# Kernel optimization log

Hardware: AMD Instinct MI355X
Metric: run time of the kernel (lower is better)

## Reference

```python
import jax, jax.numpy as jnp
import numpy as np

EPS = 1e-6
NEG = 1e9

def _norm(x):
    # Normalizator math with alpha=1, gamma=0 (torch.std is unbiased -> ddof=1)
    m = jnp.mean(x, axis=-1, keepdims=True)
    s = jnp.std(x, axis=-1, ddof=1, keepdims=True)
    return (x - m) / (s + EPS)

def setup_inputs() -> dict:
    key = jax.random.key(0)
    ks = jax.random.split(key, 16)
    T, S, D, F, L = 4096, 4096, 512, 2048, 4
    sc = 1.0 / np.sqrt(D)
    scf = 1.0 / np.sqrt(F)
    return {
        "current_tgt_output": jax.random.normal(ks[0], (T, D), jnp.float32),
        "encoder_output": jax.random.normal(ks[1], (S, D), jnp.float32),
        "cross_mask": jax.random.randint(ks[2], (T, S), 0, 2).astype(jnp.float32),
        "Wq": jax.random.normal(ks[3], (L, D, D), jnp.float32) * sc,
        "Wk": jax.random.normal(ks[4], (L, D, D), jnp.float32) * sc,
        "Wv": jax.random.normal(ks[5], (L, D, D), jnp.float32) * sc,
        "Wo": jax.random.normal(ks[6], (L, D, D), jnp.float32) * sc,
        "Cq": jax.random.normal(ks[7], (L, D, D), jnp.float32) * sc,
        "Ck": jax.random.normal(ks[8], (L, D, D), jnp.float32) * sc,
        "Cv": jax.random.normal(ks[9], (L, D, D), jnp.float32) * sc,
        "Co": jax.random.normal(ks[10], (L, D, D), jnp.float32) * sc,
        "W1": jax.random.normal(ks[11], (L, D, F), jnp.float32) * sc,
        "W2": jax.random.normal(ks[12], (L, F, D), jnp.float32) * scf,
        "alpha": jnp.ones((1,), jnp.float32),
        "gamma": jnp.zeros((1,), jnp.float32),
        "input_ids": jax.random.randint(ks[13], (T,), 0, S),
        "training_step": T,
        "training_mode": 1,
    }

def reference(current_tgt_output, encoder_output, cross_mask, Wq, Wk, Wv, Wo,
              Cq, Ck, Cv, Co, W1, W2, alpha, gamma, input_ids,
              training_step, training_mode):
    T = training_step
    x = current_tgt_output[:T] if training_mode else current_tgt_output
    cm = cross_mask[:T]                                  # [T, S]
    # the python double-loop -> single vectorized gather: self_mask[i,k]=cross_mask[i, input_ids[k]]
    self_mask = cm[:, input_ids]                         # [T, T]
    sbias = (self_mask - 1.0) * NEG                      # additive mask bias
    cbias = (cm - 1.0) * NEG
    D = x.shape[-1]
    scale = 1.0 / jnp.sqrt(jnp.asarray(D, x.dtype))
    L = Wq.shape[0]
    for l in range(L):
        h = _norm(x)
        q, k, v = h @ Wq[l], h @ Wk[l], h @ Wv[l]
        a = jax.nn.softmax(q @ k.T * scale + sbias, axis=-1)
        x = x + (a @ v) @ Wo[l]
        h = _norm(x)
        q = h @ Cq[l]
        k, v = encoder_output @ Ck[l], encoder_output @ Cv[l]
        a = jax.nn.softmax(q @ k.T * scale + cbias, axis=-1)
        x = x + (a @ v) @ Co[l]
        h = _norm(x)
        x = x + jax.nn.relu(h @ W1[l]) @ W2[l]
    return alpha * _norm(x) + gamma
```

## Files before the change

### kernel.cpp

```cpp
#include <hip/hip_runtime.h>
#include <math.h>

typedef _Float16 half_t;
typedef unsigned int u32;
typedef unsigned short u16;
typedef float f32x4 __attribute__((ext_vector_type(4)));
typedef _Float16 f16x8 __attribute__((ext_vector_type(8)));
typedef _Float16 f16x4 __attribute__((ext_vector_type(4)));

#define T_DIM 4096
#define S_DIM 4096
#define D_DIM 512
#define F_DIM 2048
#define NLAYER 4
#define KVS ((size_t)4096 * 512)

__device__ __forceinline__ void gload16(const void* g, void* l) {
    __builtin_amdgcn_global_load_lds(
        (const __attribute__((address_space(1))) u32*)g,
        (__attribute__((address_space(3))) u32*)l, 16, 0, 0);
}

template<int N> __device__ __forceinline__ void wait_vm() {
    if constexpr (N == 0) asm volatile("s_waitcnt vmcnt(0)" ::: "memory");
    else if constexpr (N == 3) asm volatile("s_waitcnt vmcnt(3)" ::: "memory");
    else if constexpr (N == 4) asm volatile("s_waitcnt vmcnt(4)" ::: "memory");
    else if constexpr (N == 6) asm volatile("s_waitcnt vmcnt(6)" ::: "memory");
    else if constexpr (N == 8) asm volatile("s_waitcnt vmcnt(8)" ::: "memory");
}

template<int BN, int EPI>
__global__ __launch_bounds__(512)
void gemm_nt(const half_t* __restrict__ A, int lda,
             const half_t* __restrict__ B, int ldb,
             int N, int K, int gx,
             half_t* __restrict__ D1, half_t* __restrict__ D2,
             half_t* __restrict__ D3, int ldd)
{
    constexpr int BM = 128, BK = 64;
    constexpr int NF = BN / 32;
    constexpr int LPT = 2 + BN / 64;
    constexpr int NSLOT = (BN == 64) ? 3 : 2;
    __shared__ half_t As[NSLOT][BM * BK];
    __shared__ half_t Bs[NSLOT][BN * BK];

    const int tid  = threadIdx.x;
    const int wave = tid >> 6;
    const int lane = tid & 63;

    const int nb  = gridDim.x;
    const int bid = blockIdx.x;
    const int nid = (bid & 7) * (nb >> 3) + (bid >> 3);
    const int bx  = nid % gx;
    const int by  = nid / gx;
    const int bm = by * BM, bn = bx * BN;

    const int wm = (wave >> 1) * 32;
    const int wn = (wave & 1) * (BN / 2);
    const int kq = lane >> 4;
    const int rr = lane & 15;
    const int scol = (((lane & 7) ^ (lane >> 3)) << 3);

    f32x4 acc[2][NF];
#pragma unroll
    for (int m = 0; m < 2; ++m)
#pragma unroll
        for (int n = 0; n < NF; ++n)
            acc[m][n] = f32x4{0.f, 0.f, 0.f, 0.f};

    auto stage = [&](int buf, int k0) {
#pragma unroll
        for (int c = 0; c < 2; ++c) {
            const int row = wave * 16 + c * 8 + (lane >> 3);
            gload16(A + (size_t)(bm + row) * lda + k0 + scol,
                    (char*)&As[buf][0] + (wave * 2 + c) * 1024 + lane * 16);
        }
        if constexpr (BN == 64) {
            const int row = wave * 8 + (lane >> 3);
            gload16(B + (size_t)(bn + row) * ldb + k0 + scol,
                    (char*)&Bs[buf][0] + wave * 1024 + lane * 16);
        } else {
#pragma unroll
            for (int c = 0; c < 2; ++c) {
                const int row = wave * 16 + c * 8 + (lane >> 3);
                gload16(B + (size_t)(bn + row) * ldb + k0 + scol,
                        (char*)&Bs[buf][0] + (wave * 2 + c) * 1024 + lane * 16);
            }
        }
    };

    const int nt = K / BK;
    stage(0, 0);
    if constexpr (NSLOT == 3) stage(1, BK);
    int cur = 0, pf = NSLOT - 1;
    for (int t = 0; t < nt; ++t) {
        if (t + 1 < nt) wait_vm<(NSLOT - 2) * LPT>(); else wait_vm<0>();
        __builtin_amdgcn_s_barrier();
        if (t + NSLOT - 1 < nt) stage(pf, (t + NSLOT - 1) * BK);
#pragma unroll
        for (int ks = 0; ks < 2; ++ks) {
            f16x8 af[2], bf[NF];
#pragma unroll
            for (int m = 0; m < 2; ++m) {
                const int r = wm + m * 16 + rr;
                af[m] = *(const f16x8*)&As[cur][r * BK + (((ks * 4 + kq) ^ (r & 7)) << 3)];
            }
#pragma unroll
            for (int n = 0; n < NF; ++n) {
                const int r = wn + n * 16 + rr;
                bf[n] = *(const f16x8*)&Bs[cur][r * BK + (((ks * 4 + kq) ^ (r & 7)) << 3)];
            }
#pragma unroll
            for (int m = 0; m < 2; ++m)
#pragma unroll
                for (int n = 0; n < NF; ++n)
                    acc[m][n] = __builtin_amdgcn_mfma_f32_16x16x32_f16(af[m], bf[n], acc[m][n], 0, 0, 0);
        }
        cur = (cur + 1 == NSLOT) ? 0 : cur + 1;
        pf  = (pf  + 1 == NSLOT) ? 0 : pf  + 1;
    }

    const int r0 = bm + wm + (lane >> 4) * 4;
#pragma unroll
    for (int m = 0; m < 2; ++m)
#pragma unroll
        for (int n = 0; n < NF; ++n) {
            const int c = bn + wn + n * 16 + rr;
            if (EPI == 2) {
#pragma unroll
                for (int i = 0; i < 4; ++i)
                    D1[(size_t)(r0 + m * 16 + i) * ldd + c] = (half_t)acc[m][n][i];
            } else if (EPI == 5) {
                half_t* Dst = (bn < 512) ? D1 : (bn < 1024) ? D2 : D3;
                const int sub = c & 511;
#pragma unroll
                for (int i = 0; i < 4; ++i)
                    Dst[(size_t)(r0 + m * 16 + i) * 512 + sub] = (half_t)acc[m][n][i];
            } else {
                const int l = c >> 10;
                const int sub = c & 1023;
                half_t* Dst = (sub < 512) ? (D2 + l * KVS) : (D3 + l * KVS);
                const int d = sub & 511;
#pragma unroll
                for (int i = 0; i < 4; ++i)
                    Dst[(size_t)(r0 + m * 16 + i) * 512 + d] = (half_t)acc[m][n][i];
            }
        }
}

__global__ __launch_bounds__(512)
void gemm_fold(const half_t* __restrict__ Wt, const half_t* __restrict__ V,
               half_t* __restrict__ Out, int zSA, long zSB, long zSD)
{
    constexpr int BM = 128, BK = 64, BN = 64, NSLOT = 3, LPT = 3;
    __shared__ half_t As[NSLOT][BM * BK];
    __shared__ half_t Bs[NSLOT][BN * BK];

    const half_t* A = Wt + (size_t)blockIdx.z * zSA;
    const half_t* B = V  + (size_t)blockIdx.z * zSB;
    half_t* D = Out + (size_t)blockIdx.z * zSD;

    const int tid  = threadIdx.x;
    const int wave = tid >> 6;
    const int lane = tid & 63;

    const int nb  = gridDim.x;
    const int bid = blockIdx.x;
    const int nid = (bid & 7) * (nb >> 3) + (bid >> 3);
    const int bx = nid & 63, by = nid >> 6;
    const int bm = by * BM, bn = bx * BN;

    const int wm = (wave >> 1) * 32;
    const int wn = (wave & 1) * 32;
    const int kq = lane >> 4;
    const int rr = lane & 15;
    const int scol = (((lane & 7) ^ (lane >> 3)) << 3);

    f32x4 acc[2][2];
#pragma unroll
    for (int m = 0; m < 2; ++m)
#pragma unroll
        for (int n = 0; n < 2; ++n)
            acc[m][n] = f32x4{0.f, 0.f, 0.f, 0.f};

    auto stage = [&](int buf, int k0) {
#pragma unroll
        for (int c = 0; c < 2; ++c) {
            const int row = wave * 16 + c * 8 + (lane >> 3);
            gload16(A + (size_t)(bm + row) * 512 + k0 + scol,
                    (char*)&As[buf][0] + (wave * 2 + c) * 1024 + lane * 16);
        }
        const int row = wave * 8 + (lane >> 3);
        gload16(B + (size_t)(bn + row) * 512 + k0 + scol,
                (char*)&Bs[buf][0] + wave * 1024 + lane * 16);
    };

    const int nt = 512 / BK;
    stage(0, 0);
    stage(1, BK);
    int cur = 0, pf = 2;
    for (int t = 0; t < nt; ++t) {
        if (t + 1 < nt) wait_vm<LPT>(); else wait_vm<0>();
        __builtin_amdgcn_s_barrier();
        if (t + 2 < nt) stage(pf, (t + 2) * BK);
#pragma unroll
        for (int ks = 0; ks < 2; ++ks) {
            f16x8 af[2], bf[2];
#pragma unroll
            for (int m = 0; m < 2; ++m) {
                const int r = wm + m * 16 + rr;
                af[m] = *(const f16x8*)&As[cur][r * BK + (((ks * 4 + kq) ^ (r & 7)) << 3)];
            }
#pragma unroll
            for (int n = 0; n < 2; ++n) {
                const int r = wn + n * 16 + rr;
                bf[n] = *(const f16x8*)&Bs[cur][r * BK + (((ks * 4 + kq) ^ (r & 7)) << 3)];
            }
#pragma unroll
            for (int m = 0; m < 2; ++m)
#pragma unroll
                for (int n = 0; n < 2; ++n)
                    acc[m][n] = __builtin_amdgcn_mfma_f32_16x16x32_f16(af[m], bf[n], acc[m][n], 0, 0, 0);
        }
        cur = (cur + 1 == NSLOT) ? 0 : cur + 1;
        pf  = (pf  + 1 == NSLOT) ? 0 : pf  + 1;
    }

    const int r0 = bm + wm + (lane >> 4) * 4;
#pragma unroll
    for (int m = 0; m < 2; ++m)
#pragma unroll
        for (int n = 0; n < 2; ++n) {
            const int c = bn + wn + n * 16 + rr;
#pragma unroll
            for (int i = 0; i < 4; ++i)
                D[(size_t)(r0 + m * 16 + i) * 4096 + c] = (half_t)acc[m][n][i];
        }
}

template<int EPI, int SPLITK = 1, int P16 = 1>
__global__ __launch_bounds__(256)
void gemm97(const half_t* __restrict__ A, int lda,
            const half_t* __restrict__ B, int ldb,
            int K, int gx, half_t* __restrict__ D,
            float* __restrict__ Fout, int ldd)
{
    constexpr int BK = 32, NSLOT = 3, LPT = 4;
    __shared__ half_t As[NSLOT][128 * BK];
    __shared__ half_t Bs[NSLOT][128 * BK];

    const int tid  = threadIdx.x;
    const int wave = tid >> 6;
    const int lane = tid & 63;

    const int nb  = gridDim.x;
    const int bid = blockIdx.x;
    const int nid = (bid & 7) * (nb >> 3) + (bid >> 3);
    const int gy  = nb / (gx * SPLITK);
    const int bx  = nid % gx;
    const int tmp = nid / gx;
    const int by  = tmp % gy;
    const int kz  = tmp / gy;
    const int bm = by * 128, bn = bx * 128;

    const int Keff = K / SPLITK;
    A += (size_t)kz * Keff;
    B += (size_t)kz * Keff;

    const int wm = (wave >> 1) * 64;
    const int wn = (wave & 1) * 64;
    const int kq = lane >> 4;
    const int rr = lane & 15;
    const int srow = lane >> 2;
    const int scol = (((lane & 3) ^ ((lane >> 3) & 3)) << 3);
    const int kqa  = kq ^ ((rr >> 1) & 3);

    const half_t* Abase = A + (size_t)(bm + wave * 16 + srow) * lda + scol;
    const half_t* Bbase = B + (size_t)(bn + wave * 16 + srow) * ldb + scol;

    f32x4 acc[4][4];
#pragma unroll
    for (int m = 0; m < 4; ++m)
#pragma unroll
        for (int n = 0; n < 4; ++n)
            acc[m][n] = f32x4{0.f, 0.f, 0.f, 0.f};

    auto stage = [&](int buf, int k0) {
#pragma unroll
        for (int c = 0; c < 2; ++c)
            gload16(Abase + (size_t)c * 64 * lda + k0,
                    (char*)&As[buf][0] + c * 4096 + wave * 1024 + lane * 16);
#pragma unroll
        for (int c = 0; c < 2; ++c)
            gload16(Bbase + (size_t)c * 64 * ldb + k0,
                    (char*)&Bs[buf][0] + c * 4096 + wave * 1024 + lane * 16);
    };

    const int nt = Keff / BK;
    stage(0, 0);
    stage(1, BK);
    int cur = 0, pf = 2;
    for (int t = 0; t < nt; ++t) {
        if (t + 1 < nt) wait_vm<LPT>(); else wait_vm<0>();
        __builtin_amdgcn_s_barrier();
        if (t + 2 < nt) stage(pf, (t + 2) * BK);
        f16x8 af[4], bf[4];
#pragma unroll
        for (int m = 0; m < 4; ++m)
            af[m] = *(const f16x8*)&As[cur][(wm + m * 16 + rr) * BK + kqa * 8];
#pragma unroll
        for (int n = 0; n < 4; ++n)
            bf[n] = *(const f16x8*)&Bs[cur][(wn + n * 16 + rr) * BK + kqa * 8];
#pragma unroll
        for (int m = 0; m < 4; ++m)
#pragma unroll
            for (int n = 0; n < 4; ++n)
                acc[m][n] = __builtin_amdgcn_mfma_f32_16x16x32_f16(af[m], bf[n], acc[m][n], 0, 0, 0);
        cur = (cur == 2) ? 0 : cur + 1;
        pf  = (pf  == 2) ? 0 : pf + 1;
    }

    const int r0 = bm + wm + (lane >> 4) * 4;
    const int soff = kz * gx * 128;
#pragma unroll
    for (int m = 0; m < 4; ++m)
#pragma unroll
        for (int n = 0; n < 4; ++n) {
            const int c = bn + wn + n * 16 + rr;
#pragma unroll
            for (int i = 0; i < 4; ++i) {
                float v = acc[m][n][i];
                const size_t r = r0 + m * 16 + i;
                if constexpr (SPLITK > 1) {
                    if constexpr (P16) D[r * ldd + soff + c] = (half_t)v;
                    else               Fout[r * ldd + soff + c] = v;
                } else {
                    if (EPI == 4) v = fmaxf(v, 0.f);
                    D[r * ldd + c] = (half_t)v;
                }
            }
        }
}

__global__ __launch_bounds__(256)
void attn_tail(const float* __restrict__ xin, const half_t* __restrict__ P,
               float* __restrict__ xbuf, half_t* __restrict__ hh)
{
    const int row  = blockIdx.x * 4 + (threadIdx.x >> 6);
    const int lane = threadIdx.x & 63;
    const int d0 = lane * 8;
    float v[8];
    {
        const float* xr = xin + (size_t)row * D_DIM + d0;
        float4 a = *(const float4*)xr;
        float4 b = *(const float4*)(xr + 4);
        v[0]=a.x; v[1]=a.y; v[2]=a.z; v[3]=a.w; v[4]=b.x; v[5]=b.y; v[6]=b.z; v[7]=b.w;
    }
    const half_t* pr = P + (size_t)row * 2048 + d0;
#pragma unroll
    for (int j = 0; j < 4; ++j) {
        f16x8 pv = *(const f16x8*)(pr + j * 512);
#pragma unroll
        for (int e = 0; e < 8; ++e) v[e] += (float)pv[e];
    }
    float* xo = xbuf + (size_t)row * D_DIM + d0;
    *(float4*)xo       = float4{v[0], v[1], v[2], v[3]};
    *(float4*)(xo + 4) = float4{v[4], v[5], v[6], v[7]};

    float s = 0.f;
#pragma unroll
    for (int j = 0; j < 8; ++j) s += v[j];
#pragma unroll
    for (int off = 32; off; off >>= 1) s += __shfl_xor(s, off);
    const float mean = s * (1.f / 512.f);
    float ss = 0.f;
#pragma unroll
    for (int j = 0; j < 8; ++j) { float d = v[j] - mean; ss += d * d; }
#pragma unroll
    for (int off = 32; off; off >>= 1) ss += __shfl_xor(ss, off);
    const float inv = 1.f / (sqrtf(ss * (1.f / 511.f)) + 1e-6f);
    f16x8 hv;
#pragma unroll
    for (int j = 0; j < 8; ++j) hv[j] = (half_t)((v[j] - mean) * inv);
    *(f16x8*)&hh[(size_t)row * D_DIM + d0] = hv;
}

template<int FINAL>
__global__ __launch_bounds__(256)
void norm_red(const float* __restrict__ xin, const float* __restrict__ P,
              float* __restrict__ xbuf, half_t* __restrict__ hh,
              float* __restrict__ outF, const float* __restrict__ alphaP,
              const float* __restrict__ gammaP)
{
    const int row  = blockIdx.x * 4 + (threadIdx.x >> 6);
    const int lane = threadIdx.x & 63;
    const int d0 = lane * 8;
    const float* xr = xin + (size_t)row * D_DIM + d0;
    float v[8];
    {
        float4 a = *(const float4*)xr;
        float4 b = *(const float4*)(xr + 4);
        v[0]=a.x; v[1]=a.y; v[2]=a.z; v[3]=a.w; v[4]=b.x; v[5]=b.y; v[6]=b.z; v[7]=b.w;
    }
    const float* pr = P + (size_t)row * 2048 + d0;
#pragma unroll
    for (int j = 0; j < 4; ++j) {
        float4 a = *(const float4*)(pr + j * 512);
        float4 b = *(const float4*)(pr + j * 512 + 4);
        v[0]+=a.x; v[1]+=a.y; v[2]+=a.z; v[3]+=a.w; v[4]+=b.x; v[5]+=b.y; v[6]+=b.z; v[7]+=b.w;
    }
    if (!FINAL) {
        float* xo = xbuf + (size_t)row * D_DIM + d0;
        *(float4*)xo       = float4{v[0], v[1], v[2], v[3]};
        *(float4*)(xo + 4) = float4{v[4], v[5], v[6], v[7]};
    }
    float s = 0.f;
#pragma unroll
    for (int j = 0; j < 8; ++j) s += v[j];
#pragma unroll
    for (int off = 32; off; off >>= 1) s += __shfl_xor(s, off);
    const float mean = s * (1.f / 512.f);
    float ss = 0.f;
#pragma unroll
    for (int j = 0; j < 8; ++j) { float d = v[j] - mean; ss += d * d; }
#pragma unroll
    for (int off = 32; off; off >>= 1) ss += __shfl_xor(ss, off);
    const float inv = 1.f / (sqrtf(ss * (1.f / 511.f)) + 1e-6f);
    if (FINAL) {
        const float alp = alphaP[0], gam = gammaP[0];
        float o[8];
#pragma unroll
        for (int j = 0; j < 8; ++j) o[j] = alp * ((v[j] - mean) * inv) + gam;
        float* op = outF + (size_t)row * D_DIM + d0;
        *(float4*)op       = float4{o[0], o[1], o[2], o[3]};
        *(float4*)(op + 4) = float4{o[4], o[5], o[6], o[7]};
    } else {
        f16x8 hv;
#pragma unroll
        for (int j = 0; j < 8; ++j) hv[j] = (half_t)((v[j] - mean) * inv);
        *(f16x8*)&hh[(size_t)row * D_DIM + d0] = hv;
    }
}

template<int FINAL>
__global__ __launch_bounds__(256)
void norm_rows(const float* __restrict__ x, half_t* __restrict__ hh,
               float* __restrict__ outF, const float* __restrict__ alphaP,
               const float* __restrict__ gammaP)
{
    const int row  = blockIdx.x * 4 + (threadIdx.x >> 6);
    const int lane = threadIdx.x & 63;
    const float* xr = x + (size_t)row * D_DIM + lane * 8;
    float4 a = *(const float4*)xr;
    float4 b = *(const float4*)(xr + 4);
    float v[8] = {a.x, a.y, a.z, a.w, b.x, b.y, b.z, b.w};
    float s = 0.f;
#pragma unroll
    for (int j = 0; j < 8; ++j) s += v[j];
#pragma unroll
    for (int off = 32; off; off >>= 1) s += __shfl_xor(s, off);
    const float mean = s * (1.f / 512.f);
    float ss = 0.f;
#pragma unroll
    for (int j = 0; j < 8; ++j) { float d = v[j] - mean; ss += d * d; }
#pragma unroll
    for (int off = 32; off; off >>= 1) ss += __shfl_xor(ss, off);
    const float inv = 1.f / (sqrtf(ss * (1.f / 511.f)) + 1e-6f);
    if (FINAL) {
        const float alp = alphaP[0], gam = gammaP[0];
        float o[8];
#pragma unroll
        for (int j = 0; j < 8; ++j) o[j] = alp * ((v[j] - mean) * inv) + gam;
        float* op = outF + (size_t)row * D_DIM + lane * 8;
        *(float4*)op       = float4{o[0], o[1], o[2], o[3]};
        *(float4*)(op + 4) = float4{o[4], o[5], o[6], o[7]};
    } else {
        f16x8 hv;
#pragma unroll
        for (int j = 0; j < 8; ++j) hv[j] = (half_t)((v[j] - mean) * inv);
        *(f16x8*)&hh[(size_t)row * D_DIM + lane * 8] = hv;
    }
}

__global__ __launch_bounds__(256)
void cast_f16(const float* __restrict__ in, half_t* __restrict__ out)
{
    size_t i = ((size_t)blockIdx.x * 256 + threadIdx.x) * 8;
    float4 a = *(const float4*)&in[i];
    float4 b = *(const float4*)&in[i + 4];
    float v[8] = {a.x, a.y, a.z, a.w, b.x, b.y, b.z, b.w};
    f16x8 o;
#pragma unroll
    for (int j = 0; j < 8; ++j) o[j] = (half_t)v[j];
    *(f16x8*)&out[i] = o;
}

__global__ __launch_bounds__(256)
void transpose_cast(const float* __restrict__ in, half_t* __restrict__ out,
                    int R, int C, float scale, int inZ, int outZ)
{
    in  += (size_t)blockIdx.z * inZ;
    out += (size_t)blockIdx.z * outZ;
    __shared__ float tile[32][33];
    const int tx = threadIdx.x & 31, ty = threadIdx.x >> 5;
    const int r0 = blockIdx.y * 32, c0 = blockIdx.x * 32;
#pragma unroll
    for (int i = 0; i < 4; ++i)
        tile[ty + i * 8][tx] = in[(size_t)(r0 + ty + i * 8) * C + c0 + tx];
    __syncthreads();
#pragma unroll
    for (int i = 0; i < 4; ++i)
        out[(size_t)(c0 + ty + i * 8) * R + r0 + tx] = (half_t)(tile[tx][ty + i * 8] * scale);
}

__global__ __launch_bounds__(256)
void pack_masks(const float* __restrict__ cm, const int* __restrict__ ids,
                u32* __restrict__ crossb, u32* __restrict__ selfb)
{
    const int t = blockIdx.x;
    const float* row = cm + (size_t)t * S_DIM;
    __shared__ u32 cb[S_DIM / 32];
    __shared__ u16 sh16[256];
    const int tid = threadIdx.x;
    u32 bits = 0;
#pragma unroll
    for (int q = 0; q < 4; ++q) {
        float4 v = *(const float4*)&row[tid * 16 + q * 4];
        bits |= (v.x > 0.5f ? 1u : 0u) << (q * 4 + 0);
        bits |= (v.y > 0.5f ? 1u : 0u) << (q * 4 + 1);
        bits |= (v.z > 0.5f ? 1u : 0u) << (q * 4 + 2);
        bits |= (v.w > 0.5f ? 1u : 0u) << (q * 4 + 3);
    }
    ((u16*)cb)[tid] = (u16)bits;
    __syncthreads();
    u32 sb = 0;
#pragma unroll
    for (int q = 0; q < 4; ++q) {
        int4 id4 = *(const int4*)&ids[tid * 16 + q * 4];
        sb |= ((cb[id4.x >> 5] >> (id4.x & 31)) & 1u) << (q * 4 + 0);
        sb |= ((cb[id4.y >> 5] >> (id4.y & 31)) & 1u) << (q * 4 + 1);
        sb |= ((cb[id4.z >> 5] >> (id4.z & 31)) & 1u) << (q * 4 + 2);
        sb |= ((cb[id4.w >> 5] >> (id4.w & 31)) & 1u) << (q * 4 + 3);
    }
    sh16[tid] = (u16)sb;
    __syncthreads();
    if (tid < 128) {
        crossb[(size_t)t * 128 + tid] = cb[tid];
        selfb[(size_t)t * 128 + tid]  = (u32)sh16[2 * tid] | ((u32)sh16[2 * tid + 1] << 16);
    }
}

__global__ __launch_bounds__(256)
void softmax_rows16(half_t* __restrict__ logits, const u32* __restrict__ bits)
{
    const int t = blockIdx.x;
    half_t* row = logits + (size_t)t * S_DIM;
    const u32* bw = bits + (size_t)t * (S_DIM / 32);
    __shared__ float red[8];
    const int tid = threadIdx.x, wave = tid >> 6, lane = tid & 63;
    const int s0 = tid * 16;
    f16x8 h0 = *(const f16x8*)&row[s0];
    f16x8 h1 = *(const f16x8*)&row[s0 + 8];
    const u32 w = bw[tid >> 1] >> ((tid & 1) * 16);
    float z[16];
    float lmax = -3.0e38f;
#pragma unroll
    for (int q = 0; q < 16; ++q) {
        const float v = (float)((q < 8) ? h0[q & 7] : h1[q & 7]);
        z[q] = v + (((w >> q) & 1u) ? 0.f : -1e9f);
        lmax = fmaxf(lmax, z[q]);
    }
#pragma unroll
    for (int off = 32; off; off >>= 1) lmax = fmaxf(lmax, __shfl_xor(lmax, off));
    if (lane == 0) red[wave] = lmax;
    __syncthreads();
    const float mx = fmaxf(fmaxf(red[0], red[1]), fmaxf(red[2], red[3]));
    float lsum = 0.f;
#pragma unroll
    for (int q = 0; q < 16; ++q) { z[q] = __expf(z[q] - mx); lsum += z[q]; }
#pragma unroll
    for (int off = 32; off; off >>= 1) lsum += __shfl_xor(lsum, off);
    if (lane == 0) red[4 + wave] = lsum;
    __syncthreads();
    const float inv = 1.f / (red[4] + red[5] + red[6] + red[7]);
    f16x8 o0, o1;
#pragma unroll
    for (int q = 0; q < 8; ++q) {
        o0[q] = (half_t)(z[q] * inv);
        o1[q] = (half_t)(z[q + 8] * inv);
    }
    *(f16x8*)&row[s0] = o0;
    *(f16x8*)&row[s0 + 8] = o1;
}

extern "C" void kernel_launch(void* const* d_in, const int* in_sizes, int n_in,
                              void* d_out, int out_size, void* d_ws, size_t ws_size,
                              hipStream_t stream)
{
    (void)in_sizes; (void)n_in; (void)out_size; (void)ws_size;

    const float* x0p  = (const float*)d_in[0];
    const float* encp = (const float*)d_in[1];
    const float* cmp  = (const float*)d_in[2];
    const float* Wq = (const float*)d_in[3], *Wk = (const float*)d_in[4];
    const float* Wv = (const float*)d_in[5], *Wo = (const float*)d_in[6];
    const float* Cq = (const float*)d_in[7], *Ck = (const float*)d_in[8];
    const float* Cv = (const float*)d_in[9], *Co = (const float*)d_in[10];
    const float* W1p = (const float*)d_in[11];
    const float* W2p = (const float*)d_in[12];
    const float* alphap = (const float*)d_in[13];
    const float* gammap = (const float*)d_in[14];
    const int*   idsp   = (const int*)d_in[15];
    float* outp = (float*)d_out;

    char* wp = (char*)d_ws;
    auto take = [&](size_t nelem, int esz) -> void* {
        void* p = (void*)wp;
        wp += (nelem * (size_t)esz + 255) & ~(size_t)255;
        return p;
    };
    half_t* wqkvT = (half_t*)take((size_t)NLAYER * 1536 * 512, 2);
    half_t* ckvT  = (half_t*)take((size_t)NLAYER * 1024 * 512, 2);
    half_t* cqT   = (half_t*)take((size_t)NLAYER * 512 * 512, 2);
    half_t* woT   = (half_t*)take((size_t)NLAYER * 512 * 512, 2);
    half_t* coT   = (half_t*)take((size_t)NLAYER * 512 * 512, 2);
    half_t* w1T   = (half_t*)take((size_t)NLAYER * D_DIM * F_DIM, 2);
    half_t* w2T   = (half_t*)take((size_t)NLAYER * D_DIM * F_DIM, 2);
    half_t* hh    = (half_t*)take((size_t)T_DIM * D_DIM, 2);
    half_t* qb    = (half_t*)take((size_t)T_DIM * D_DIM, 2);
    half_t* kb    = (half_t*)take((size_t)S_DIM * D_DIM, 2);
    half_t* vb    = (half_t*)take((size_t)S_DIM * D_DIM, 2);
    half_t* vTp   = (half_t*)take((size_t)S_DIM * D_DIM, 2);
    half_t* mid   = (half_t*)take((size_t)T_DIM * F_DIM, 2);
    half_t* enc16 = (half_t*)take((size_t)S_DIM * D_DIM, 2);
    half_t* kbC   = (half_t*)take((size_t)NLAYER * S_DIM * D_DIM, 2);
    half_t* vC    = (half_t*)take((size_t)NLAYER * S_DIM * D_DIM, 2);
    half_t* vTCp  = (half_t*)take((size_t)NLAYER * S_DIM * D_DIM, 2);
    float* xbuf   = (float*)take((size_t)T_DIM * D_DIM, 4);
    half_t* logit16 = (half_t*)take((size_t)T_DIM * S_DIM, 2);
    half_t* p16   = (half_t*)take((size_t)T_DIM * 2048, 2);
    float* pbuf   = (float*)take((size_t)T_DIM * 2048, 4);
    u32* crossb = (u32*)take((size_t)T_DIM * (S_DIM / 32), 4);
    u32* selfb  = (u32*)take((size_t)T_DIM * (S_DIM / 32), 4);

    const dim3 B(256), B512(512);
    const float qscale = 0.04419417382415922f;

    const int SQ = 512 * 512, QKVZ = 1536 * 512, KVZ = 1024 * 512, FZ = 512 * 2048;
    transpose_cast<<<dim3(16,16,4), B, 0, stream>>>(Wq, wqkvT,            512, 512, qscale, SQ, QKVZ);
    transpose_cast<<<dim3(16,16,4), B, 0, stream>>>(Wk, wqkvT + SQ,       512, 512, 1.f,    SQ, QKVZ);
    transpose_cast<<<dim3(16,16,4), B, 0, stream>>>(Wv, wqkvT + 2 * SQ,   512, 512, 1.f,    SQ, QKVZ);
    transpose_cast<<<dim3(16,16,4), B, 0, stream>>>(Wo, woT,              512, 512, 1.f,    SQ, SQ);
    transpose_cast<<<dim3(16,16,4), B, 0, stream>>>(Cq, cqT,              512, 512, qscale, SQ, SQ);
    transpose_cast<<<dim3(16,16,4), B, 0, stream>>>(Ck, ckvT,             512, 512, 1.f,    SQ, KVZ);
    transpose_cast<<<dim3(16,16,4), B, 0, stream>>>(Cv, ckvT + SQ,        512, 512, 1.f,    SQ, KVZ);
    transpose_cast<<<dim3(16,16,4), B, 0, stream>>>(Co, coT,              512, 512, 1.f,    SQ, SQ);
    transpose_cast<<<dim3(64,16,4), B, 0, stream>>>(W1p, w1T, 512, 2048, 1.f, FZ, FZ);
    transpose_cast<<<dim3(16,64,4), B, 0, stream>>>(W2p, w2T, 2048, 512, 1.f, FZ, FZ);
    cast_f16<<<dim3((S_DIM * D_DIM / 8) / 256), B, 0, stream>>>(encp, enc16);
    pack_masks<<<dim3(T_DIM), B, 0, stream>>>(cmp, idsp, crossb, selfb);
    gemm_nt<64, 7><<<dim3(2048), B512, 0, stream>>>(enc16, 512, ckvT, 512,
        4096, 512, 64, nullptr, kbC, vC, 0);
    gemm_fold<<<dim3(256, 1, NLAYER), B512, 0, stream>>>(coT, vC, vTCp,
        SQ, (long)KVS, (long)KVS);

    for (int l = 0; l < NLAYER; ++l) {
        if (l == 0)
            norm_rows<0><<<T_DIM / 4, B, 0, stream>>>(x0p, hh, nullptr, nullptr, nullptr);
        else
            norm_red<0><<<T_DIM / 4, B, 0, stream>>>(xbuf, pbuf, xbuf, hh, nullptr, nullptr, nullptr);

        gemm_nt<64, 5><<<dim3(768), B512, 0, stream>>>(hh, 512, wqkvT + (size_t)l * QKVZ, 512,
            1536, 512, 24, qb, kb, vb, 0);
        gemm_fold<<<dim3(256, 1, 1), B512, 0, stream>>>(woT + (size_t)l * SQ, vb, vTp, 0, 0, 0);
        gemm97<2><<<dim3(1024), B, 0, stream>>>(qb, 512, kb, 512, 512, 32, logit16, nullptr, 4096);
        softmax_rows16<<<dim3(T_DIM), B, 0, stream>>>(logit16, selfb);
        gemm97<0, 4, 1><<<dim3(512), B, 0, stream>>>(logit16, 4096, vTp, 4096,
            4096, 4, p16, nullptr, 2048);
        attn_tail<<<dim3(T_DIM / 4), B, 0, stream>>>((l == 0) ? x0p : xbuf, p16, xbuf, hh);

        gemm_nt<64, 2><<<dim3(256), B512, 0, stream>>>(hh, 512, cqT + (size_t)l * SQ, 512,
            512, 512, 8, qb, nullptr, nullptr, 512);
        gemm97<2><<<dim3(1024), B, 0, stream>>>(qb, 512, kbC + (size_t)l * KVS, 512,
            512, 32, logit16, nullptr, 4096);
        softmax_rows16<<<dim3(T_DIM), B, 0, stream>>>(logit16, crossb);
        gemm97<0, 4, 1><<<dim3(512), B, 0, stream>>>(logit16, 4096, vTCp + (size_t)l * KVS, 4096,
            4096, 4, p16, nullptr, 2048);
        attn_tail<<<dim3(T_DIM / 4), B, 0, stream>>>(xbuf, p16, xbuf, hh);

        gemm97<4><<<dim3(512), B, 0, stream>>>(hh, 512, w1T + (size_t)l * FZ, 512,
            512, 16, mid, nullptr, 2048);
        gemm97<0, 4, 0><<<dim3(512), B, 0, stream>>>(mid, 2048, w2T + (size_t)l * FZ, 2048,
            2048, 4, nullptr, pbuf, 2048);
    }

    norm_red<1><<<T_DIM / 4, B, 0, stream>>>(xbuf, pbuf, xbuf, nullptr, outp, alphap, gammap);
}
```

Baseline: 1.100 ms.

## Fuse masked softmax into logits GEMM epilogue and PV GEMM prologue

The separate softmax pass over the 4096x4096 fp16 logits is removed. The logits GEMM now applies the mask bits, writes raw masked logits, and emits per-tile row max and sum statistics. A small combine kernel merges these into a per-row max and inverse sum. The PV GEMM then loads logits through registers, applies exp and normalisation before staging them in LDS, and uses direct-to-LDS loads only for V. This saves one full read and write of the logits matrix per attention, at the cost of extra epilogue reductions, exp work inside the GEMM main loop, and a register-staged A path.

```diff
diff --git a/kernel.cpp b/kernel.cpp
--- a/kernel.cpp
+++ b/kernel.cpp
@@ -27,6 +27,9 @@
     else if constexpr (N == 4) asm volatile("s_waitcnt vmcnt(4)" ::: "memory");
     else if constexpr (N == 6) asm volatile("s_waitcnt vmcnt(6)" ::: "memory");
     else if constexpr (N == 8) asm volatile("s_waitcnt vmcnt(8)" ::: "memory");
+}
+__device__ __forceinline__ void wait_lgkm0() {
+    asm volatile("s_waitcnt lgkmcnt(0)" ::: "memory");
 }
 
 template<int BN, int EPI>
@@ -343,6 +346,300 @@
 }
 
 __global__ __launch_bounds__(256)
+void gemm_logits(const half_t* __restrict__ A, const half_t* __restrict__ B,
+                 const u32* __restrict__ bits, half_t* __restrict__ D,
+                 float2* __restrict__ stats)
+{
+    constexpr int BK = 32, NSLOT = 3, LPT = 4, nt = 16;
+    __shared__ half_t As[NSLOT][128 * BK];
+    __shared__ half_t Bs[NSLOT][128 * BK];
+    __shared__ float sred[2][128][2];
+
+    const int tid  = threadIdx.x;
+    const int wave = tid >> 6;
+    const int lane = tid & 63;
+
+    const int nb  = gridDim.x;
+    const int bid = blockIdx.x;
+    const int nid = (bid & 7) * (nb >> 3) + (bid >> 3);
+    const int bx = nid & 31, by = nid >> 5;
+    const int bm = by * 128, bn = bx * 128;
+
+    const int wm = (wave >> 1) * 64;
+    const int wn = (wave & 1) * 64;
+    const int kq = lane >> 4;
+    const int rr = lane & 15;
+    const int srow = lane >> 2;
+    const int scol = (((lane & 3) ^ ((lane >> 3) & 3)) << 3);
+    const int kqa  = kq ^ ((rr >> 1) & 3);
+
+    const half_t* Abase = A + (size_t)(bm + wave * 16 + srow) * 512 + scol;
+    const half_t* Bbase = B + (size_t)(bn + wave * 16 + srow) * 512 + scol;
+
+    f32x4 acc[4][4];
+#pragma unroll
+    for (int m = 0; m < 4; ++m)
+#pragma unroll
+        for (int n = 0; n < 4; ++n)
+            acc[m][n] = f32x4{0.f, 0.f, 0.f, 0.f};
+
+    auto stage = [&](int buf, int k0) {
+#pragma unroll
+        for (int c = 0; c < 2; ++c)
+            gload16(Abase + (size_t)c * 64 * 512 + k0,
+                    (char*)&As[buf][0] + c * 4096 + wave * 1024 + lane * 16);
+#pragma unroll
+        for (int c = 0; c < 2; ++c)
+            gload16(Bbase + (size_t)c * 64 * 512 + k0,
+                    (char*)&Bs[buf][0] + c * 4096 + wave * 1024 + lane * 16);
+    };
+
+    stage(0, 0);
+    stage(1, BK);
+    int cur = 0, pf = 2;
+    for (int t = 0; t < nt; ++t) {
+        if (t + 1 < nt) wait_vm<LPT>(); else wait_vm<0>();
+        __builtin_amdgcn_s_barrier();
+        if (t + 2 < nt) stage(pf, (t + 2) * BK);
+        f16x8 af[4], bf[4];
+#pragma unroll
+        for (int m = 0; m < 4; ++m)
+            af[m] = *(const f16x8*)&As[cur][(wm + m * 16 + rr) * BK + kqa * 8];
+#pragma unroll
+        for (int n = 0; n < 4; ++n)
+            bf[n] = *(const f16x8*)&Bs[cur][(wn + n * 16 + rr) * BK + kqa * 8];
+#pragma unroll
+        for (int m = 0; m < 4; ++m)
+#pragma unroll
+            for (int n = 0; n < 4; ++n)
+                acc[m][n] = __builtin_amdgcn_mfma_f32_16x16x32_f16(af[m], bf[n], acc[m][n], 0, 0, 0);
+        cur = (cur == 2) ? 0 : cur + 1;
+        pf  = (pf  == 2) ? 0 : pf + 1;
+    }
+
+    const int g4 = (lane >> 4) * 4;
+    const int r0 = bm + wm + g4;
+    const int wordbase = (bn + wn) >> 5;
+    float rmax[4][4];
+#pragma unroll
+    for (int m = 0; m < 4; ++m)
+#pragma unroll
+        for (int i = 0; i < 4; ++i) {
+            const int r = r0 + m * 16 + i;
+            const u32 w01 = bits[(size_t)r * 128 + wordbase];
+            const u32 w23 = bits[(size_t)r * 128 + wordbase + 1];
+#pragma unroll
+            for (int n = 0; n < 4; ++n) {
+                const u32 w = (n < 2) ? w01 : w23;
+                const u32 bit = (w >> ((n & 1) * 16 + rr)) & 1u;
+                acc[m][n][i] += bit ? 0.f : -1e9f;
+            }
+            rmax[m][i] = fmaxf(fmaxf(acc[m][0][i], acc[m][1][i]),
+                               fmaxf(acc[m][2][i], acc[m][3][i]));
+        }
+#pragma unroll
+    for (int m = 0; m < 4; ++m)
+#pragma unroll
+        for (int i = 0; i < 4; ++i)
+#pragma unroll
+            for (int off = 1; off < 16; off <<= 1)
+                rmax[m][i] = fmaxf(rmax[m][i], __shfl_xor(rmax[m][i], off));
+    if (rr == 0) {
+#pragma unroll
+        for (int m = 0; m < 4; ++m)
+#pragma unroll
+            for (int i = 0; i < 4; ++i)
+                sred[0][wm + g4 + m * 16 + i][wave & 1] = rmax[m][i];
+    }
+    __syncthreads();
+    float rsum[4][4];
+#pragma unroll
+    for (int m = 0; m < 4; ++m)
+#pragma unroll
+        for (int i = 0; i < 4; ++i) {
+            const int rl = wm + g4 + m * 16 + i;
+            const float M = fmaxf(sred[0][rl][0], sred[0][rl][1]);
+            rmax[m][i] = M;
+            float s = 0.f;
+#pragma unroll
+            for (int n = 0; n < 4; ++n) s += __expf(acc[m][n][i] - M);
+            rsum[m][i] = s;
+        }
+#pragma unroll
+    for (int m = 0; m < 4; ++m)
+#pragma unroll
+        for (int i = 0; i < 4; ++i)
+#pragma unroll
+            for (int off = 1; off < 16; off <<= 1)
+                rsum[m][i] += __shfl_xor(rsum[m][i], off);
+    if (rr == 0) {
+#pragma unroll
+        for (int m = 0; m < 4; ++m)
+#pragma unroll
+            for (int i = 0; i < 4; ++i)
+                sred[1][wm + g4 + m * 16 + i][wave & 1] = rsum[m][i];
+    }
+    __syncthreads();
+#pragma unroll
+    for (int m = 0; m < 4; ++m)
+#pragma unroll
+        for (int n = 0; n < 4; ++n) {
+            const int c = bn + wn + n * 16 + rr;
+#pragma unroll
+            for (int i = 0; i < 4; ++i)
+                D[(size_t)(r0 + m * 16 + i) * 4096 + c] = (half_t)acc[m][n][i];
+        }
+    if (rr == 0 && (wave & 1) == 0) {
+#pragma unroll
+        for (int m = 0; m < 4; ++m)
+#pragma unroll
+            for (int i = 0; i < 4; ++i) {
+                const int rl = wm + g4 + m * 16 + i;
+                stats[(size_t)(bm + rl) * 32 + bx] =
+                    float2{rmax[m][i], sred[1][rl][0] + sred[1][rl][1]};
+            }
+    }
+}
+
+__global__ __launch_bounds__(256)
+void softmax_combine(const float2* __restrict__ stats, float2* __restrict__ rowstat)
+{
+    const int row = blockIdx.x * 8 + (threadIdx.x >> 5);
+    const int t = threadIdx.x & 31;
+    const float2 st = stats[(size_t)row * 32 + t];
+    float M = st.x;
+#pragma unroll
+    for (int off = 16; off; off >>= 1) M = fmaxf(M, __shfl_xor(M, off));
+    float s = st.y * __expf(st.x - M);
+#pragma unroll
+    for (int off = 16; off; off >>= 1) s += __shfl_xor(s, off);
+    if (t == 0) rowstat[row] = float2{M, 1.f / s};
+}
+
+__global__ __launch_bounds__(256)
+void gemm_pv(const half_t* __restrict__ A, const half_t* __restrict__ B,
+             const float2* __restrict__ rowstat, half_t* __restrict__ D)
+{
+    constexpr int BK = 32, NSLOT = 3, Keff = 1024, nt = 32;
+    __shared__ half_t As[NSLOT][128 * BK];
+    __shared__ half_t Bs[NSLOT][128 * BK];
+
+    const int tid = threadIdx.x, wave = tid >> 6, lane = tid & 63;
+    const int nb = gridDim.x, bid = blockIdx.x;
+    const int nid = (bid & 7) * (nb >> 3) + (bid >> 3);
+    const int bx = nid & 3;
+    const int tmp = nid >> 2;
+    const int by = tmp & 31, kz = tmp >> 5;
+    const int bm = by * 128, bn = bx * 128;
+
+    const int wm = (wave >> 1) * 64, wn = (wave & 1) * 64;
+    const int kq = lane >> 4, rr = lane & 15, srow = lane >> 2;
+    const int scol = (((lane & 3) ^ ((lane >> 3) & 3)) << 3);
+    const int kqa = kq ^ ((rr >> 1) & 3);
+
+    const int arow = bm + wave * 16 + srow;
+    const half_t* Abase = A + (size_t)arow * 4096 + kz * Keff + scol;
+    const half_t* Bbase = B + (size_t)(bn + wave * 16 + srow) * 4096 + kz * Keff + scol;
+
+    const float2 rs0 = rowstat[arow];
+    const float2 rs1 = rowstat[arow + 64];
+    asm volatile("s_waitcnt vmcnt(0)" ::: "memory");
+    const float M0 = rs0.x, I0 = rs0.y, M1 = rs1.x, I1 = rs1.y;
+
+    f32x4 acc[4][4];
+#pragma unroll
+    for (int m = 0; m < 4; ++m)
+#pragma unroll
+        for (int n = 0; n < 4; ++n)
+            acc[m][n] = f32x4{0.f, 0.f, 0.f, 0.f};
+
+    auto loadA = [&](int k0, f16x8& a0, f16x8& a1) {
+        a0 = *(const f16x8*)(Abase + k0);
+        a1 = *(const f16x8*)(Abase + (size_t)64 * 4096 + k0);
+    };
+    auto gloadB = [&](int buf, int k0) {
+        gload16(Bbase + k0, (char*)&Bs[buf][0] + wave * 1024 + lane * 16);
+        gload16(Bbase + (size_t)64 * 4096 + k0,
+                (char*)&Bs[buf][0] + 4096 + wave * 1024 + lane * 16);
+    };
+    auto writeA = [&](int buf, const f16x8& a0, const f16x8& a1) {
+        f16x8 p0, p1;
+#pragma unroll
+        for (int e = 0; e < 8; ++e) {
+            p0[e] = (half_t)(__expf((float)a0[e] - M0) * I0);
+            p1[e] = (half_t)(__expf((float)a1[e] - M1) * I1);
+        }
+        *(f16x8*)((char*)&As[buf][0] + wave * 1024 + lane * 16) = p0;
+        *(f16x8*)((char*)&As[buf][0] + 4096 + wave * 1024 + lane * 16) = p1;
+    };
+    auto compute = [&](int s) {
+        f16x8 af[4], bf[4];
+#pragma unroll
+        for (int m = 0; m < 4; ++m)
+            af[m] = *(const f16x8*)&As[s][(wm + m * 16 + rr) * BK + kqa * 8];
+#pragma unroll
+        for (int n = 0; n < 4; ++n)
+            bf[n] = *(const f16x8*)&Bs[s][(wn + n * 16 + rr) * BK + kqa * 8];
+#pragma unroll
+        for (int m = 0; m < 4; ++m)
+#pragma unroll
+            for (int n = 0; n < 4; ++n)
+                acc[m][n] = __builtin_amdgcn_mfma_f32_16x16x32_f16(af[m], bf[n], acc[m][n], 0, 0, 0);
+    };
+
+    f16x8 a0A, a1A, a0B, a1B;
+    loadA(0, a0A, a1A);  gloadB(0, 0);
+    loadA(BK, a0B, a1B); gloadB(1, BK);
+    wait_vm<4>();
+    writeA(0, a0A, a1A);
+    wait_lgkm0();
+    __builtin_amdgcn_s_barrier();
+
+    int cur = 0, pf = 2;
+    for (int t = 0; t < nt; t += 2) {
+        {
+            const bool hasPF = (t + 2 < nt);
+            if (hasPF) { loadA((t + 2) * BK, a0A, a1A); gloadB(pf, (t + 2) * BK); }
+            compute(cur);
+            if (t + 1 < nt) {
+                if (hasPF) wait_vm<4>(); else wait_vm<0>();
+                writeA((cur + 1 == NSLOT) ? 0 : cur + 1, a0B, a1B);
+                wait_lgkm0();
+            }
+            __builtin_amdgcn_s_barrier();
+            cur = (cur + 1 == NSLOT) ? 0 : cur + 1;
+            pf  = (pf  + 1 == NSLOT) ? 0 : pf + 1;
+        }
+        {
+            const int u = t + 1;
+            const bool hasPF = (u + 2 < nt);
+            if (hasPF) { loadA((u + 2) * BK, a0B, a1B); gloadB(pf, (u + 2) * BK); }
+            compute(cur);
+            if (u + 1 < nt) {
+                if (hasPF) wait_vm<4>(); else wait_vm<0>();
+                writeA((cur + 1 == NSLOT) ? 0 : cur + 1, a0A, a1A);
+                wait_lgkm0();
+            }
+            __builtin_amdgcn_s_barrier();
+            cur = (cur + 1 == NSLOT) ? 0 : cur + 1;
+            pf  = (pf  + 1 == NSLOT) ? 0 : pf + 1;
+        }
+    }
+
+    const int r0 = bm + wm + (lane >> 4) * 4;
+    const int soff = kz * 512;
+#pragma unroll
+    for (int m = 0; m < 4; ++m)
+#pragma unroll
+        for (int n = 0; n < 4; ++n) {
+            const int c = bn + wn + n * 16 + rr;
+#pragma unroll
+            for (int i = 0; i < 4; ++i)
+                D[(size_t)(r0 + m * 16 + i) * 2048 + soff + c] = (half_t)acc[m][n][i];
+        }
+}
+
+__global__ __launch_bounds__(256)
 void attn_tail(const float* __restrict__ xin, const half_t* __restrict__ P,
                float* __restrict__ xbuf, half_t* __restrict__ hh)
 {
@@ -548,49 +845,6 @@
         crossb[(size_t)t * 128 + tid] = cb[tid];
         selfb[(size_t)t * 128 + tid]  = (u32)sh16[2 * tid] | ((u32)sh16[2 * tid + 1] << 16);
     }
-}
-
-__global__ __launch_bounds__(256)
-void softmax_rows16(half_t* __restrict__ logits, const u32* __restrict__ bits)
-{
-    const int t = blockIdx.x;
-    half_t* row = logits + (size_t)t * S_DIM;
-    const u32* bw = bits + (size_t)t * (S_DIM / 32);
-    __shared__ float red[8];
-    const int tid = threadIdx.x, wave = tid >> 6, lane = tid & 63;
-    const int s0 = tid * 16;
-    f16x8 h0 = *(const f16x8*)&row[s0];
-    f16x8 h1 = *(const f16x8*)&row[s0 + 8];
-    const u32 w = bw[tid >> 1] >> ((tid & 1) * 16);
-    float z[16];
-    float lmax = -3.0e38f;
-#pragma unroll
-    for (int q = 0; q < 16; ++q) {
-        const float v = (float)((q < 8) ? h0[q & 7] : h1[q & 7]);
-        z[q] = v + (((w >> q) & 1u) ? 0.f : -1e9f);
-        lmax = fmaxf(lmax, z[q]);
-    }
-#pragma unroll
-    for (int off = 32; off; off >>= 1) lmax = fmaxf(lmax, __shfl_xor(lmax, off));
-    if (lane == 0) red[wave] = lmax;
-    __syncthreads();
-    const float mx = fmaxf(fmaxf(red[0], red[1]), fmaxf(red[2], red[3]));
-    float lsum = 0.f;
-#pragma unroll
-    for (int q = 0; q < 16; ++q) { z[q] = __expf(z[q] - mx); lsum += z[q]; }
-#pragma unroll
-    for (int off = 32; off; off >>= 1) lsum += __shfl_xor(lsum, off);
-    if (lane == 0) red[4 + wave] = lsum;
-    __syncthreads();
-    const float inv = 1.f / (red[4] + red[5] + red[6] + red[7]);
-    f16x8 o0, o1;
-#pragma unroll
-    for (int q = 0; q < 8; ++q) {
-        o0[q] = (half_t)(z[q] * inv);
-        o1[q] = (half_t)(z[q + 8] * inv);
-    }
-    *(f16x8*)&row[s0] = o0;
-    *(f16x8*)&row[s0 + 8] = o1;
 }
 
 extern "C" void kernel_launch(void* const* d_in, const int* in_sizes, int n_in,
@@ -640,6 +894,8 @@
     half_t* logit16 = (half_t*)take((size_t)T_DIM * S_DIM, 2);
     half_t* p16   = (half_t*)take((size_t)T_DIM * 2048, 2);
     float* pbuf   = (float*)take((size_t)T_DIM * 2048, 4);
+    float2* statsS = (float2*)take((size_t)T_DIM * 32, 8);
+    float2* rowstat = (float2*)take((size_t)T_DIM, 8);
     u32* crossb = (u32*)take((size_t)T_DIM * (S_DIM / 32), 4);
     u32* selfb  = (u32*)take((size_t)T_DIM * (S_DIM / 32), 4);
 
@@ -673,19 +929,16 @@
         gemm_nt<64, 5><<<dim3(768), B512, 0, stream>>>(hh, 512, wqkvT + (size_t)l * QKVZ, 512,
             1536, 512, 24, qb, kb, vb, 0);
         gemm_fold<<<dim3(256, 1, 1), B512, 0, stream>>>(woT + (size_t)l * SQ, vb, vTp, 0, 0, 0);
-        gemm97<2><<<dim3(1024), B, 0, stream>>>(qb, 512, kb, 512, 512, 32, logit16, nullptr, 4096);
-        softmax_rows16<<<dim3(T_DIM), B, 0, stream>>>(logit16, selfb);
-        gemm97<0, 4, 1><<<dim3(512), B, 0, stream>>>(logit16, 4096, vTp, 4096,
-            4096, 4, p16, nullptr, 2048);
+        gemm_logits<<<dim3(1024), B, 0, stream>>>(qb, kb, selfb, logit16, statsS);
+        softmax_combine<<<dim3(512), B, 0, stream>>>(statsS, rowstat);
+        gemm_pv<<<dim3(512), B, 0, stream>>>(logit16, vTp, rowstat, p16);
         attn_tail<<<dim3(T_DIM / 4), B, 0, stream>>>((l == 0) ? x0p : xbuf, p16, xbuf, hh);
 
         gemm_nt<64, 2><<<dim3(256), B512, 0, stream>>>(hh, 512, cqT + (size_t)l * SQ, 512,
             512, 512, 8, qb, nullptr, nullptr, 512);
-        gemm97<2><<<dim3(1024), B, 0, stream>>>(qb, 512, kbC + (size_t)l * KVS, 512,
-            512, 32, logit16, nullptr, 4096);
-        softmax_rows16<<<dim3(T_DIM), B, 0, stream>>>(logit16, crossb);
-        gemm97<0, 4, 1><<<dim3(512), B, 0, stream>>>(logit16, 4096, vTCp + (size_t)l * KVS, 4096,
-            4096, 4, p16, nullptr, 2048);
+        gemm_logits<<<dim3(1024), B, 0, stream>>>(qb, kbC + (size_t)l * KVS, crossb, logit16, statsS);
+        softmax_combine<<<dim3(512), B, 0, stream>>>(statsS, rowstat);
+        gemm_pv<<<dim3(512), B, 0, stream>>>(logit16, vTCp + (size_t)l * KVS, rowstat, p16);
         attn_tail<<<dim3(T_DIM / 4), B, 0, stream>>>(xbuf, p16, xbuf, hh);
 
         gemm97<4><<<dim3(512), B, 0, stream>>>(hh, 512, w1T + (size_t)l * FZ, 512,
```

Result: slower. 1.291 ms (+17.3%).
